# Kernel tuning notes

Measured on AMD Instinct MI355X. Metric: run time of the kernel, lower is better.

Reference implementation:

```python
import jax, jax.numpy as jnp
import numpy as np

N, E, D, L = 50000, 640000, 128, 3  # nodes, edges, channels, layers
EPS = 1e-5


def setup_inputs() -> dict:
    key = jax.random.key(0)
    ks = jax.random.split(key, 10)
    s = 1.0 / np.sqrt(D)
    inp = {
        "x": jax.random.normal(ks[0], (N, D), dtype=jnp.float32),
        "edge_attr": jax.random.normal(ks[1], (E, D), dtype=jnp.float32),
        "w_self": jax.random.normal(ks[2], (L, D, D), dtype=jnp.float32) * s,
        "b_self": jnp.zeros((L, D), dtype=jnp.float32),
        "w_in": jax.random.normal(ks[3], (L, D, D), dtype=jnp.float32) * s,
        "b_in": jnp.zeros((L, D), dtype=jnp.float32),
        "w_rel": jax.random.normal(ks[4], (L, D, D), dtype=jnp.float32) * s,
        "b_rel": jnp.zeros((L, D), dtype=jnp.float32),
        "bn_gamma": jnp.ones((L - 1, D), dtype=jnp.float32),
        "bn_beta": jnp.zeros((L - 1, D), dtype=jnp.float32),
        "edge_index": jax.random.randint(ks[5], (2, E), 0, N, dtype=jnp.int64),
    }
    return inp


def _batchnorm(h, gamma, beta):
    mu = jnp.mean(h, axis=0)
    var = jnp.mean(jnp.square(h - mu), axis=0)  # biased var (torch BN training)
    return (h - mu) * jax.lax.rsqrt(var + EPS) * gamma + beta


def reference(x, edge_attr, w_self, b_self, w_in, b_in, w_rel, b_rel,
              bn_gamma, bn_beta, edge_index):
    src, dst = edge_index[0], edge_index[1]
    # per-node in-degree for mean aggregation (zero-degree nodes -> 0)
    cnt = jax.ops.segment_sum(jnp.ones((E, 1), x.dtype), dst, num_segments=N)
    denom = jnp.maximum(cnt, 1.0)
    for i in range(L):
        # message: lin_in(x_j * edge_attr)
        msg = jnp.einsum('ed,fd->ef', x[src] * edge_attr, w_in[i]) + b_in[i]
        agg = jax.ops.segment_sum(msg, dst, num_segments=N) / denom  # scatter-mean
        x = agg + jnp.einsum('nd,fd->nf', x, w_self[i]) + b_self[i]
        edge_attr = jnp.einsum('ed,fd->ef', edge_attr, w_rel[i]) + b_rel[i]
        if i < L - 1:
            x = jax.nn.relu(_batchnorm(x, bn_gamma[i], bn_beta[i]))
            # dropout p=0.0 -> identity
    return (x, edge_attr)
```

## Files before the change

kernel.cpp:

```cpp
#include <hip/hip_runtime.h>

#define DD 128

typedef __attribute__((ext_vector_type(8))) short bf16x8;
typedef __attribute__((ext_vector_type(4))) short bf16x4;
typedef __attribute__((ext_vector_type(4))) float f32x4;
typedef unsigned short u16;

__device__ __forceinline__ unsigned short f2bf(float f) {
  union { float f; unsigned u; } v; v.f = f;
  unsigned u = v.u;
  return (unsigned short)((u + 0x7FFFu + ((u >> 16) & 1u)) >> 16);
}
__device__ __forceinline__ float bf2f(unsigned short h) {
  union { unsigned u; float f; } v; v.u = ((unsigned)h) << 16; return v.f;
}
__device__ __forceinline__ bf16x8 pack8(f32x4 a, f32x4 b) {
  bf16x8 r;
  r[0] = (short)f2bf(a.x); r[1] = (short)f2bf(a.y);
  r[2] = (short)f2bf(a.z); r[3] = (short)f2bf(a.w);
  r[4] = (short)f2bf(b.x); r[5] = (short)f2bf(b.y);
  r[6] = (short)f2bf(b.z); r[7] = (short)f2bf(b.w);
  return r;
}

__device__ __forceinline__ bool idx_is64(const int* p) {
  return (p[1] | p[3] | p[5] | p[7]) == 0;
}
__device__ __forceinline__ int ld_idx(const int* p, long long i, bool is64) {
  return is64 ? (int)((const long long*)p)[i] : p[i];
}

__global__ void k_count(const int* __restrict__ idx, int* __restrict__ cnt, int E) {
  int e = blockIdx.x * blockDim.x + threadIdx.x;
  if (e >= E) return;
  bool is64 = idx_is64(idx);
  int d = ld_idx(idx, (long long)E + e, is64);
  atomicAdd(&cnt[d], 1);
}

__global__ __launch_bounds__(1024) void k_scan(const int* __restrict__ cnt,
    int* __restrict__ row_start, int* __restrict__ cursor, int N) {
  __shared__ int part[1024];
  int t = threadIdx.x;
  int chunk = (N + 1023) >> 10;
  int lo = t * chunk, hi = lo + chunk; if (hi > N) hi = N; if (lo > N) lo = N;
  int s = 0;
  for (int i = lo; i < hi; ++i) s += cnt[i];
  part[t] = s;
  __syncthreads();
  for (int off = 1; off < 1024; off <<= 1) {
    int v = (t >= off) ? part[t - off] : 0;
    __syncthreads();
    part[t] += v;
    __syncthreads();
  }
  int run = (t == 0) ? 0 : part[t - 1];
  for (int i = lo; i < hi; ++i) {
    row_start[i] = run; cursor[i] = run; run += cnt[i];
  }
  if (t == 1023) row_start[N] = part[1023];
}

__global__ void k_fill(const int* __restrict__ idx, int* __restrict__ cursor,
                       int* __restrict__ edge_of, int* __restrict__ src_csr, int E) {
  int e = blockIdx.x * blockDim.x + threadIdx.x;
  if (e >= E) return;
  bool is64 = idx_is64(idx);
  int s = ld_idx(idx, e, is64);
  int d = ld_idx(idx, (long long)E + e, is64);
  int pos = atomicAdd(&cursor[d], 1);
  edge_of[pos] = e;
  src_csr[pos] = s;
}

template <int MODE>
__global__ __launch_bounds__(256, 4) void k_ar(
    const float* __restrict__ x0, const u16* __restrict__ xbin,
    const float* __restrict__ ea0, const u16* __restrict__ eain,
    u16* __restrict__ eabout, float* __restrict__ eafout,
    float* __restrict__ aggmf, u16* __restrict__ aggm,
    const int* __restrict__ row_start, const int* __restrict__ edge_of,
    const int* __restrict__ src_csr,
    const float* __restrict__ w_rel, const float* __restrict__ b_rel,
    const float* __restrict__ scale, const float* __restrict__ shift,
    int nA, int ntE) {
  __shared__ short Wl[16384];
  int bid = blockIdx.x;
  int tid = threadIdx.x;
  int wave = tid >> 6, lane = tid & 63;
  (void)aggmf;

  if (bid < nA) {
    int n = bid * 4 + wave;
    int esub = lane >> 4, cg = lane & 15;
    int c0 = cg * 8;
    float scA[8], shA[8];
    if constexpr (MODE >= 1) {
#pragma unroll
      for (int j = 0; j < 8; ++j) { scA[j] = scale[c0 + j]; shA[j] = shift[c0 + j]; }
    }
    int s0 = row_start[n], s1 = row_start[n + 1];
    int len = s1 - s0;
    float acc[8];
#pragma unroll
    for (int j = 0; j < 8; ++j) acc[j] = 0.f;
    for (int kk = 0; kk < len; kk += 8) {
      int kx0 = kk + esub, kx1 = kk + 4 + esub;
      bool a0 = kx0 < len, a1 = kx1 < len;
      int k0 = s0 + (a0 ? kx0 : 0);
      int k1 = s0 + (a1 ? kx1 : 0);
      if constexpr (MODE == 0) {
        int e0 = edge_of[k0], e1 = edge_of[k1];
        int sn0 = src_csr[k0], sn1 = src_csr[k1];
        const float* ep0 = ea0 + (size_t)e0 * DD + c0;
        const float* ep1 = ea0 + (size_t)e1 * DD + c0;
        const float* xp0 = x0 + (size_t)sn0 * DD + c0;
        const float* xp1 = x0 + (size_t)sn1 * DD + c0;
        f32x4 ea0a = *(const f32x4*)ep0, ea0b = *(const f32x4*)(ep0 + 4);
        f32x4 ea1a = *(const f32x4*)ep1, ea1b = *(const f32x4*)(ep1 + 4);
        f32x4 xv0a = *(const f32x4*)xp0, xv0b = *(const f32x4*)(xp0 + 4);
        f32x4 xv1a = *(const f32x4*)xp1, xv1b = *(const f32x4*)(xp1 + 4);
        if (a0) {
#pragma unroll
          for (int j = 0; j < 4; ++j) { acc[j] += xv0a[j] * ea0a[j]; acc[4 + j] += xv0b[j] * ea0b[j]; }
        }
        if (a1) {
#pragma unroll
          for (int j = 0; j < 4; ++j) { acc[j] += xv1a[j] * ea1a[j]; acc[4 + j] += xv1b[j] * ea1b[j]; }
        }
      } else {
        int sn0 = src_csr[k0], sn1 = src_csr[k1];
        bf16x8 ev0 = *(const bf16x8*)(eain + (size_t)k0 * DD + c0);
        bf16x8 ev1 = *(const bf16x8*)(eain + (size_t)k1 * DD + c0);
        bf16x8 xv0 = *(const bf16x8*)(xbin + (size_t)sn0 * DD + c0);
        bf16x8 xv1 = *(const bf16x8*)(xbin + (size_t)sn1 * DD + c0);
        if (a0) {
#pragma unroll
          for (int j = 0; j < 8; ++j) {
            float xf = fmaxf(bf2f((u16)xv0[j]) * scA[j] + shA[j], 0.f);
            acc[j] += xf * bf2f((u16)ev0[j]);
          }
        }
        if (a1) {
#pragma unroll
          for (int j = 0; j < 8; ++j) {
            float xf = fmaxf(bf2f((u16)xv1[j]) * scA[j] + shA[j], 0.f);
            acc[j] += xf * bf2f((u16)ev1[j]);
          }
        }
      }
    }
    float invd = (len > 0) ? 1.0f / (float)len : 0.0f;
#pragma unroll
    for (int j = 0; j < 8; ++j) {
      float s = acc[j];
      s += __shfl_xor(s, 16);
      s += __shfl_xor(s, 32);
      acc[j] = s * invd;
    }
    if (esub == 0) {
      f32x4 lo, hi;
#pragma unroll
      for (int j = 0; j < 4; ++j) { lo[j] = acc[j]; hi[j] = acc[4 + j]; }
      *(bf16x8*)(aggm + (size_t)n * DD + c0) = pack8(lo, hi);
    }
  } else {
    for (int q = tid; q < 4096; q += 256) {
      int off = q * 4;
      int f = off >> 7, d = off & 127;
      f32x4 w = *(const f32x4*)(w_rel + off);
      unsigned byte = ((unsigned)(f * 256 + d * 2)) ^ (unsigned)((f & 7) << 4);
      bf16x4 s4;
      s4[0] = (short)f2bf(w.x); s4[1] = (short)f2bf(w.y);
      s4[2] = (short)f2bf(w.z); s4[3] = (short)f2bf(w.w);
      *(bf16x4*)((char*)Wl + byte) = s4;
    }
    __syncthreads();
    int r = lane & 15, g = lane >> 4;
    int tile = (bid - nA) * 4 + wave;
    if (tile >= ntE) return;
    bf16x8 a8[4];
    if constexpr (MODE == 0) {
      int er = edge_of[tile * 16 + r];
      const float* rp = ea0 + (size_t)er * DD;
#pragma unroll
      for (int ks = 0; ks < 4; ++ks) {
        const float* p = rp + ks * 32 + g * 8;
        a8[ks] = pack8(*(const f32x4*)p, *(const f32x4*)(p + 4));
      }
    } else {
      const u16* rp = eain + (size_t)(tile * 16 + r) * DD;
#pragma unroll
      for (int ks = 0; ks < 4; ++ks) a8[ks] = *(const bf16x8*)(rp + ks * 32 + g * 8);
    }
    f32x4 acc4[8];
#pragma unroll
    for (int ct = 0; ct < 8; ++ct) acc4[ct] = (f32x4){0.f, 0.f, 0.f, 0.f};
#pragma unroll
    for (int ct = 0; ct < 8; ++ct) {
      int f = ct * 16 + r;
      unsigned base = (unsigned)(f * 256);
      unsigned sw = (unsigned)((f & 7) << 4);
#pragma unroll
      for (int ks = 0; ks < 4; ++ks) {
        unsigned byte = (base + (unsigned)(ks * 64 + g * 16)) ^ sw;
        bf16x8 bb = *(const bf16x8*)((const char*)Wl + byte);
        acc4[ct] = __builtin_amdgcn_mfma_f32_16x16x32_bf16(a8[ks], bb, acc4[ct], 0, 0, 0);
      }
    }
    size_t orow[4];
#pragma unroll
    for (int j = 0; j < 4; ++j) {
      int kr = tile * 16 + g * 4 + j;
      if constexpr (MODE == 2) orow[j] = (size_t)edge_of[kr];
      else                     orow[j] = (size_t)kr;
    }
#pragma unroll
    for (int ct = 0; ct < 8; ++ct) {
      int col = ct * 16 + r;
      float bv = b_rel[col];
#pragma unroll
      for (int j = 0; j < 4; ++j) {
        float v = acc4[ct][j] + bv;
        if constexpr (MODE == 2) eafout[orow[j] * DD + col] = v;
        else                     eabout[orow[j] * DD + col] = f2bf(v);
      }
    }
  }
}

template <typename TX, bool BN, typename TO, bool STATS>
__global__ __launch_bounds__(256, 2) void k_node(const u16* __restrict__ aggm,
    const TX* __restrict__ xc, const float* __restrict__ W_in,
    const float* __restrict__ W_self, const float* __restrict__ b_in,
    const float* __restrict__ b_self, const int* __restrict__ row_start,
    const float* __restrict__ scale, const float* __restrict__ shift,
    TO* __restrict__ xn, float* __restrict__ gsum, float* __restrict__ gssq,
    int ntiles) {
  __shared__ short Wl[DD * 256];
  for (int q = threadIdx.x; q < DD * 256 / 4; q += 256) {
    int off = q * 4;
    int f = off >> 8, k = off & 255;
    f32x4 w = (k < 128) ? *(const f32x4*)(W_in + f * 128 + k)
                        : *(const f32x4*)(W_self + f * 128 + (k - 128));
    unsigned byte = ((unsigned)(f * 512 + k * 2)) ^ (unsigned)((f & 7) << 4);
    bf16x4 s4;
    s4[0] = (short)f2bf(w.x); s4[1] = (short)f2bf(w.y);
    s4[2] = (short)f2bf(w.z); s4[3] = (short)f2bf(w.w);
    *(bf16x4*)((char*)Wl + byte) = s4;
  }
  __syncthreads();
  int wave = threadIdx.x >> 6, lane = threadIdx.x & 63;
  int tile = blockIdx.x * 4 + wave;
  if (tile >= ntiles) return;
  int r = lane & 15, g = lane >> 4;
  int arowi = tile * 16 + r;
  const u16* arow = aggm + (size_t)arowi * DD;
  const TX* xrow = xc + (size_t)arowi * DD;
  bf16x8 a[8];
#pragma unroll
  for (int ks = 0; ks < 4; ++ks) a[ks] = *(const bf16x8*)(arow + ks * 32 + g * 8);
#pragma unroll
  for (int ks = 0; ks < 4; ++ks) {
    int c0 = ks * 32 + g * 8;
    if constexpr (sizeof(TX) == 2) {
      bf16x8 raw = *(const bf16x8*)(xrow + c0);
      bf16x8 fr;
#pragma unroll
      for (int j = 0; j < 8; ++j) {
        float f = bf2f((u16)raw[j]);
        if constexpr (BN) f = fmaxf(f * scale[c0 + j] + shift[c0 + j], 0.f);
        fr[j] = (short)f2bf(f);
      }
      a[4 + ks] = fr;
    } else {
      const float* p = (const float*)xrow + c0;
      a[4 + ks] = pack8(*(const f32x4*)p, *(const f32x4*)(p + 4));
    }
  }
  f32x4 acc[8];
#pragma unroll
  for (int ct = 0; ct < 8; ++ct) acc[ct] = (f32x4){0.f, 0.f, 0.f, 0.f};
#pragma unroll
  for (int ct = 0; ct < 8; ++ct) {
    int f = ct * 16 + r;
    unsigned base = (unsigned)(f * 512);
    unsigned sw = (unsigned)((f & 7) << 4);
#pragma unroll
    for (int ks = 0; ks < 8; ++ks) {
      unsigned byte = (base + (unsigned)(ks * 64 + g * 16)) ^ sw;
      bf16x8 b = *(const bf16x8*)((const char*)Wl + byte);
      acc[ct] = __builtin_amdgcn_mfma_f32_16x16x32_bf16(a[ks], b, acc[ct], 0, 0, 0);
    }
  }
  int nbase = tile * 16;
  float degmask[4];
#pragma unroll
  for (int j = 0; j < 4; ++j) {
    int nn = nbase + g * 4 + j;
    degmask[j] = (row_start[nn + 1] > row_start[nn]) ? 1.0f : 0.0f;
  }
#pragma unroll
  for (int ct = 0; ct < 8; ++ct) {
    int col = ct * 16 + r;
    float bi = b_in[col], bs = b_self[col];
    float s = 0.f, s2 = 0.f;
#pragma unroll
    for (int j = 0; j < 4; ++j) {
      float v = acc[ct][j] + bs + bi * degmask[j];
      if constexpr (sizeof(TO) == 2) xn[(size_t)(nbase + g * 4 + j) * DD + col] = (TO)f2bf(v);
      else                            xn[(size_t)(nbase + g * 4 + j) * DD + col] = (TO)v;
      s += v; s2 += v * v;
    }
    if constexpr (STATS) {
      s += __shfl_xor(s, 16);  s += __shfl_xor(s, 32);
      s2 += __shfl_xor(s2, 16); s2 += __shfl_xor(s2, 32);
      if (g == 0) { atomicAdd(&gsum[col], s); atomicAdd(&gssq[col], s2); }
    }
  }
}

__global__ void k_bnfin(float* __restrict__ gsum, float* __restrict__ gssq,
    const float* __restrict__ gamma, const float* __restrict__ beta,
    float* __restrict__ scale, float* __restrict__ shift, int N) {
  int d = threadIdx.x;
  float mu = gsum[d] / (float)N;
  float var = gssq[d] / (float)N - mu * mu;
  float rs = rsqrtf(var + 1e-5f);
  float sc = rs * gamma[d];
  scale[d] = sc;
  shift[d] = beta[d] - mu * sc;
  gsum[d] = 0.f;
  gssq[d] = 0.f;
}

static inline size_t alignup(size_t v, size_t a) { return (v + a - 1) & ~(a - 1); }

extern "C" void kernel_launch(void* const* d_in, const int* in_sizes, int n_in,
                              void* d_out, int out_size, void* d_ws, size_t ws_size,
                              hipStream_t stream) {
  const float* x0     = (const float*)d_in[0];
  const float* ea0    = (const float*)d_in[1];
  const float* w_self = (const float*)d_in[2];
  const float* b_self = (const float*)d_in[3];
  const float* w_in   = (const float*)d_in[4];
  const float* b_in   = (const float*)d_in[5];
  const float* w_rel  = (const float*)d_in[6];
  const float* b_rel  = (const float*)d_in[7];
  const float* gamma  = (const float*)d_in[8];
  const float* beta   = (const float*)d_in[9];
  const int*   idx    = (const int*)d_in[10];

  const int N = in_sizes[0] / DD;
  const int E = in_sizes[1] / DD;

  char* w = (char*)d_ws;
  size_t off = 0;
  int* cnt       = (int*)(w + off); off = alignup(off + (size_t)N * 4, 256);
  int* row_start = (int*)(w + off); off = alignup(off + (size_t)(N + 1) * 4, 256);
  int* cursor    = (int*)(w + off); off = alignup(off + (size_t)N * 4, 256);
  int* edge_of   = (int*)(w + off); off = alignup(off + (size_t)E * 4, 256);
  int* src_csr   = (int*)(w + off); off = alignup(off + (size_t)E * 4, 256);
  float* gstats  = (float*)(w + off); off = alignup(off + 256 * 4, 256);
  float* scale   = (float*)(w + off); off = alignup(off + 128 * 4, 256);
  float* shift   = (float*)(w + off); off = alignup(off + 128 * 4, 256);
  u16* aggm      = (u16*)(w + off); off = alignup(off + (size_t)N * DD * 2, 256);
  u16* xbA       = (u16*)(w + off); off = alignup(off + (size_t)N * DD * 2, 256);
  u16* xbB       = (u16*)(w + off); off = alignup(off + (size_t)N * DD * 2, 256);
  u16* eaA       = (u16*)(w + off); off = alignup(off + (size_t)E * DD * 2, 256);
  u16* eaB       = (u16*)(w + off); off = alignup(off + (size_t)E * DD * 2, 256);
  float* gsum = gstats, *gssq = gstats + 128;
  (void)ws_size; (void)n_in; (void)out_size;

  float* out_x  = (float*)d_out;
  float* out_ea = out_x + (size_t)N * DD;

  (void)hipMemsetAsync(cnt, 0, (size_t)N * 4, stream);
  int ethreads = 256, eblocks = (E + ethreads - 1) / ethreads;
  k_count<<<eblocks, ethreads, 0, stream>>>(idx, cnt, E);
  k_scan<<<1, 1024, 0, stream>>>(cnt, row_start, cursor, N);
  k_fill<<<eblocks, ethreads, 0, stream>>>(idx, cursor, edge_of, src_csr, E);
  (void)hipMemsetAsync(gstats, 0, 256 * 4, stream);

  const int ntN = N / 16;
  const int ntE = E / 16;
  const int nA = (N + 3) / 4;
  const int nB = (ntE + 3) / 4;
  const int grid = nA + nB;
  const int nodeBlocks = (ntN + 3) / 4;

  k_ar<0><<<grid, 256, 0, stream>>>(x0, nullptr, ea0, nullptr,
      eaA, nullptr, nullptr, aggm, row_start, edge_of, src_csr,
      w_rel, b_rel, scale, shift, nA, ntE);
  k_node<float, false, u16, true><<<nodeBlocks, 256, 0, stream>>>(aggm, x0,
      w_in, w_self, b_in, b_self, row_start, scale, shift,
      xbA, gsum, gssq, ntN);
  k_bnfin<<<1, 128, 0, stream>>>(gsum, gssq, gamma, beta, scale, shift, N);

  k_ar<1><<<grid, 256, 0, stream>>>(nullptr, xbA, nullptr, eaA,
      eaB, nullptr, nullptr, aggm, row_start, edge_of, src_csr,
      w_rel + DD * DD, b_rel + DD, scale, shift, nA, ntE);
  k_node<u16, true, u16, true><<<nodeBlocks, 256, 0, stream>>>(aggm, xbA,
      w_in + DD * DD, w_self + DD * DD, b_in + DD, b_self + DD,
      row_start, scale, shift, xbB, gsum, gssq, ntN);
  k_bnfin<<<1, 128, 0, stream>>>(gsum, gssq, gamma + DD, beta + DD, scale, shift, N);

  k_ar<2><<<grid, 256, 0, stream>>>(nullptr, xbB, nullptr, eaB,
      nullptr, out_ea, nullptr, aggm, row_start, edge_of, src_csr,
      w_rel + 2 * DD * DD, b_rel + 2 * DD, scale, shift, nA, ntE);
  k_node<u16, true, float, false><<<nodeBlocks, 256, 0, stream>>>(aggm, xbB,
      w_in + 2 * DD * DD, w_self + 2 * DD * DD, b_in + 2 * DD, b_self + 2 * DD,
      row_start, scale, shift, out_x, gsum, gssq, ntN);
}
```

Measured before the change: 1.029 ms.

## Fuse edge aggregation into edge-update MFMA pass with segmented scan and atomics

Replaces the split node-gather / edge-GEMM kernel with a single edge-parallel kernel. Each wave loads an edge's attributes and source features once and uses them both for the w_rel MFMA and for the message product. Messages are reduced per destination with a segmented shuffle scan, written to an fp32 aggregation buffer with plain stores when a segment lies inside the wave's range and atomics otherwise. BatchNorm+ReLU moves into a separate elementwise pass that writes a post-activation bf16 copy. The cost is an extra fp32 N×D buffer that must be memset each layer, 32-float register carries and lower occupancy (launch bounds cut from 4 to 2), plus atomic contention on high-degree nodes.

```diff
diff --git a/kernel.cpp b/kernel.cpp
--- a/kernel.cpp
+++ b/kernel.cpp
@@ -63,7 +63,8 @@
 }
 
 __global__ void k_fill(const int* __restrict__ idx, int* __restrict__ cursor,
-                       int* __restrict__ edge_of, int* __restrict__ src_csr, int E) {
+                       int* __restrict__ edge_of, int* __restrict__ src_csr,
+                       int* __restrict__ dst_csr, int E) {
   int e = blockIdx.x * blockDim.x + threadIdx.x;
   if (e >= E) return;
   bool is64 = idx_is64(idx);
@@ -72,131 +73,82 @@
   int pos = atomicAdd(&cursor[d], 1);
   edge_of[pos] = e;
   src_csr[pos] = s;
+  dst_csr[pos] = d;
 }
 
 template <int MODE>
-__global__ __launch_bounds__(256, 4) void k_ar(
-    const float* __restrict__ x0, const u16* __restrict__ xbin,
+__global__ __launch_bounds__(256, 2) void k_layer(
+    const float* __restrict__ x0, const u16* __restrict__ xpin,
     const float* __restrict__ ea0, const u16* __restrict__ eain,
     u16* __restrict__ eabout, float* __restrict__ eafout,
-    float* __restrict__ aggmf, u16* __restrict__ aggm,
+    float* __restrict__ aggsum,
     const int* __restrict__ row_start, const int* __restrict__ edge_of,
-    const int* __restrict__ src_csr,
+    const int* __restrict__ src_csr, const int* __restrict__ dst_csr,
     const float* __restrict__ w_rel, const float* __restrict__ b_rel,
-    const float* __restrict__ scale, const float* __restrict__ shift,
-    int nA, int ntE) {
+    int E) {
   __shared__ short Wl[16384];
-  int bid = blockIdx.x;
-  int tid = threadIdx.x;
-  int wave = tid >> 6, lane = tid & 63;
-  (void)aggmf;
-
-  if (bid < nA) {
-    int n = bid * 4 + wave;
-    int esub = lane >> 4, cg = lane & 15;
-    int c0 = cg * 8;
-    float scA[8], shA[8];
-    if constexpr (MODE >= 1) {
-#pragma unroll
-      for (int j = 0; j < 8; ++j) { scA[j] = scale[c0 + j]; shA[j] = shift[c0 + j]; }
-    }
-    int s0 = row_start[n], s1 = row_start[n + 1];
-    int len = s1 - s0;
-    float acc[8];
-#pragma unroll
-    for (int j = 0; j < 8; ++j) acc[j] = 0.f;
-    for (int kk = 0; kk < len; kk += 8) {
-      int kx0 = kk + esub, kx1 = kk + 4 + esub;
-      bool a0 = kx0 < len, a1 = kx1 < len;
-      int k0 = s0 + (a0 ? kx0 : 0);
-      int k1 = s0 + (a1 ? kx1 : 0);
-      if constexpr (MODE == 0) {
-        int e0 = edge_of[k0], e1 = edge_of[k1];
-        int sn0 = src_csr[k0], sn1 = src_csr[k1];
-        const float* ep0 = ea0 + (size_t)e0 * DD + c0;
-        const float* ep1 = ea0 + (size_t)e1 * DD + c0;
-        const float* xp0 = x0 + (size_t)sn0 * DD + c0;
-        const float* xp1 = x0 + (size_t)sn1 * DD + c0;
-        f32x4 ea0a = *(const f32x4*)ep0, ea0b = *(const f32x4*)(ep0 + 4);
-        f32x4 ea1a = *(const f32x4*)ep1, ea1b = *(const f32x4*)(ep1 + 4);
-        f32x4 xv0a = *(const f32x4*)xp0, xv0b = *(const f32x4*)(xp0 + 4);
-        f32x4 xv1a = *(const f32x4*)xp1, xv1b = *(const f32x4*)(xp1 + 4);
-        if (a0) {
-#pragma unroll
-          for (int j = 0; j < 4; ++j) { acc[j] += xv0a[j] * ea0a[j]; acc[4 + j] += xv0b[j] * ea0b[j]; }
+  for (int q = threadIdx.x; q < 4096; q += 256) {
+    int off = q * 4;
+    int f = off >> 7, d = off & 127;
+    f32x4 w = *(const f32x4*)(w_rel + off);
+    unsigned byte = ((unsigned)(f * 256 + d * 2)) ^ (unsigned)((f & 7) << 4);
+    bf16x4 s4;
+    s4[0] = (short)f2bf(w.x); s4[1] = (short)f2bf(w.y);
+    s4[2] = (short)f2bf(w.z); s4[3] = (short)f2bf(w.w);
+    *(bf16x4*)((char*)Wl + byte) = s4;
+  }
+  __syncthreads();
+  int wid = blockIdx.x * 4 + (threadIdx.x >> 6);
+  int wk0 = wid * 64;
+  if (wk0 >= E) return;
+  int lane = threadIdx.x & 63, r = lane & 15, g = lane >> 4;
+
+  float carry[32];
+  int cdst = -1;
+#pragma unroll
+  for (int ch = 0; ch < 32; ++ch) carry[ch] = 0.f;
+
+#pragma unroll 1
+  for (int st = 0; st < 4; ++st) {
+    int k0 = wk0 + st * 16;
+    int kr = k0 + r;
+    int dr = dst_csr[kr];
+    int sn = src_csr[kr];
+    bf16x8 a8[4];
+    float m[32];
+    if constexpr (MODE == 0) {
+      int e = edge_of[kr];
+      const float* ep = ea0 + (size_t)e * DD;
+      const float* xp = x0 + (size_t)sn * DD;
+#pragma unroll
+      for (int ks = 0; ks < 4; ++ks) {
+        int c0 = ks * 32 + g * 8;
+        f32x4 e0 = *(const f32x4*)(ep + c0), e1 = *(const f32x4*)(ep + c0 + 4);
+        f32x4 xv0 = *(const f32x4*)(xp + c0), xv1 = *(const f32x4*)(xp + c0 + 4);
+        a8[ks] = pack8(e0, e1);
+#pragma unroll
+        for (int j = 0; j < 4; ++j) {
+          m[ks * 8 + j] = e0[j] * xv0[j];
+          m[ks * 8 + 4 + j] = e1[j] * xv1[j];
         }
-        if (a1) {
-#pragma unroll
-          for (int j = 0; j < 4; ++j) { acc[j] += xv1a[j] * ea1a[j]; acc[4 + j] += xv1b[j] * ea1b[j]; }
-        }
-      } else {
-        int sn0 = src_csr[k0], sn1 = src_csr[k1];
-        bf16x8 ev0 = *(const bf16x8*)(eain + (size_t)k0 * DD + c0);
-        bf16x8 ev1 = *(const bf16x8*)(eain + (size_t)k1 * DD + c0);
-        bf16x8 xv0 = *(const bf16x8*)(xbin + (size_t)sn0 * DD + c0);
-        bf16x8 xv1 = *(const bf16x8*)(xbin + (size_t)sn1 * DD + c0);
-        if (a0) {
-#pragma unroll
-          for (int j = 0; j < 8; ++j) {
-            float xf = fmaxf(bf2f((u16)xv0[j]) * scA[j] + shA[j], 0.f);
-            acc[j] += xf * bf2f((u16)ev0[j]);
-          }
-        }
-        if (a1) {
-#pragma unroll
-          for (int j = 0; j < 8; ++j) {
-            float xf = fmaxf(bf2f((u16)xv1[j]) * scA[j] + shA[j], 0.f);
-            acc[j] += xf * bf2f((u16)ev1[j]);
-          }
-        }
-      }
-    }
-    float invd = (len > 0) ? 1.0f / (float)len : 0.0f;
-#pragma unroll
-    for (int j = 0; j < 8; ++j) {
-      float s = acc[j];
-      s += __shfl_xor(s, 16);
-      s += __shfl_xor(s, 32);
-      acc[j] = s * invd;
-    }
-    if (esub == 0) {
-      f32x4 lo, hi;
-#pragma unroll
-      for (int j = 0; j < 4; ++j) { lo[j] = acc[j]; hi[j] = acc[4 + j]; }
-      *(bf16x8*)(aggm + (size_t)n * DD + c0) = pack8(lo, hi);
-    }
-  } else {
-    for (int q = tid; q < 4096; q += 256) {
-      int off = q * 4;
-      int f = off >> 7, d = off & 127;
-      f32x4 w = *(const f32x4*)(w_rel + off);
-      unsigned byte = ((unsigned)(f * 256 + d * 2)) ^ (unsigned)((f & 7) << 4);
-      bf16x4 s4;
-      s4[0] = (short)f2bf(w.x); s4[1] = (short)f2bf(w.y);
-      s4[2] = (short)f2bf(w.z); s4[3] = (short)f2bf(w.w);
-      *(bf16x4*)((char*)Wl + byte) = s4;
-    }
-    __syncthreads();
-    int r = lane & 15, g = lane >> 4;
-    int tile = (bid - nA) * 4 + wave;
-    if (tile >= ntE) return;
-    bf16x8 a8[4];
-    if constexpr (MODE == 0) {
-      int er = edge_of[tile * 16 + r];
-      const float* rp = ea0 + (size_t)er * DD;
+      }
+    } else {
+      const u16* ep = eain + (size_t)kr * DD;
+      const u16* xp = xpin + (size_t)sn * DD;
 #pragma unroll
       for (int ks = 0; ks < 4; ++ks) {
-        const float* p = rp + ks * 32 + g * 8;
-        a8[ks] = pack8(*(const f32x4*)p, *(const f32x4*)(p + 4));
-      }
-    } else {
-      const u16* rp = eain + (size_t)(tile * 16 + r) * DD;
-#pragma unroll
-      for (int ks = 0; ks < 4; ++ks) a8[ks] = *(const bf16x8*)(rp + ks * 32 + g * 8);
-    }
-    f32x4 acc4[8];
-#pragma unroll
-    for (int ct = 0; ct < 8; ++ct) acc4[ct] = (f32x4){0.f, 0.f, 0.f, 0.f};
+        int c0 = ks * 32 + g * 8;
+        bf16x8 ev = *(const bf16x8*)(ep + c0);
+        bf16x8 xv = *(const bf16x8*)(xp + c0);
+        a8[ks] = ev;
+#pragma unroll
+        for (int j = 0; j < 8; ++j)
+          m[ks * 8 + j] = bf2f((u16)ev[j]) * bf2f((u16)xv[j]);
+      }
+    }
+    f32x4 acc[8];
+#pragma unroll
+    for (int ct = 0; ct < 8; ++ct) acc[ct] = (f32x4){0.f, 0.f, 0.f, 0.f};
 #pragma unroll
     for (int ct = 0; ct < 8; ++ct) {
       int f = ct * 16 + r;
@@ -206,15 +158,15 @@
       for (int ks = 0; ks < 4; ++ks) {
         unsigned byte = (base + (unsigned)(ks * 64 + g * 16)) ^ sw;
         bf16x8 bb = *(const bf16x8*)((const char*)Wl + byte);
-        acc4[ct] = __builtin_amdgcn_mfma_f32_16x16x32_bf16(a8[ks], bb, acc4[ct], 0, 0, 0);
+        acc[ct] = __builtin_amdgcn_mfma_f32_16x16x32_bf16(a8[ks], bb, acc[ct], 0, 0, 0);
       }
     }
     size_t orow[4];
 #pragma unroll
     for (int j = 0; j < 4; ++j) {
-      int kr = tile * 16 + g * 4 + j;
-      if constexpr (MODE == 2) orow[j] = (size_t)edge_of[kr];
-      else                     orow[j] = (size_t)kr;
+      int kk = k0 + g * 4 + j;
+      if constexpr (MODE == 2) orow[j] = (size_t)edge_of[kk];
+      else                     orow[j] = (size_t)kk;
     }
 #pragma unroll
     for (int ct = 0; ct < 8; ++ct) {
@@ -222,20 +174,105 @@
       float bv = b_rel[col];
 #pragma unroll
       for (int j = 0; j < 4; ++j) {
-        float v = acc4[ct][j] + bv;
+        float v = acc[ct][j] + bv;
         if constexpr (MODE == 2) eafout[orow[j] * DD + col] = v;
         else                     eabout[orow[j] * DD + col] = f2bf(v);
       }
     }
-  }
-}
-
-template <typename TX, bool BN, typename TO, bool STATS>
-__global__ __launch_bounds__(256, 2) void k_node(const u16* __restrict__ aggm,
+    int d0 = __shfl(dr, 0, 16);
+    if (cdst >= 0 && cdst != d0) {
+      if (r == 0) {
+        int s0d = row_start[cdst], s1d = row_start[cdst + 1];
+        bool cont = (s0d >= wk0) && (s1d <= wk0 + 64);
+        float* dp = aggsum + (size_t)cdst * DD;
+        if (cont) {
+#pragma unroll
+          for (int ks = 0; ks < 4; ++ks) {
+            f32x4 lo, hi;
+#pragma unroll
+            for (int j = 0; j < 4; ++j) { lo[j] = carry[ks * 8 + j]; hi[j] = carry[ks * 8 + 4 + j]; }
+            *(f32x4*)(dp + ks * 32 + g * 8) = lo;
+            *(f32x4*)(dp + ks * 32 + g * 8 + 4) = hi;
+          }
+        } else {
+#pragma unroll
+          for (int ks = 0; ks < 4; ++ks)
+#pragma unroll
+            for (int j = 0; j < 8; ++j)
+              unsafeAtomicAdd(dp + ks * 32 + g * 8 + j, carry[ks * 8 + j]);
+        }
+      }
+      cdst = -1;
+    }
+#pragma unroll
+    for (int s = 1; s < 16; s <<= 1) {
+      int dprev = __shfl_up(dr, s, 16);
+      bool take = (r >= s) && (dprev == dr);
+#pragma unroll
+      for (int ch = 0; ch < 32; ++ch) {
+        float v = __shfl_up(m[ch], s, 16);
+        m[ch] += take ? v : 0.f;
+      }
+    }
+    if (dr == cdst) {
+#pragma unroll
+      for (int ch = 0; ch < 32; ++ch) m[ch] += carry[ch];
+    }
+    int dnext = __shfl_down(dr, 1, 16);
+    bool tail = (r < 15) && (dnext != dr);
+    if (tail) {
+      int s0d = row_start[dr], s1d = row_start[dr + 1];
+      bool cont = (s0d >= wk0) && (s1d <= wk0 + 64);
+      float* dp = aggsum + (size_t)dr * DD;
+      if (cont) {
+#pragma unroll
+        for (int ks = 0; ks < 4; ++ks) {
+          f32x4 lo, hi;
+#pragma unroll
+          for (int j = 0; j < 4; ++j) { lo[j] = m[ks * 8 + j]; hi[j] = m[ks * 8 + 4 + j]; }
+          *(f32x4*)(dp + ks * 32 + g * 8) = lo;
+          *(f32x4*)(dp + ks * 32 + g * 8 + 4) = hi;
+        }
+      } else {
+#pragma unroll
+        for (int ks = 0; ks < 4; ++ks)
+#pragma unroll
+          for (int j = 0; j < 8; ++j)
+            unsafeAtomicAdd(dp + ks * 32 + g * 8 + j, m[ks * 8 + j]);
+      }
+    }
+#pragma unroll
+    for (int ch = 0; ch < 32; ++ch) carry[ch] = __shfl(m[ch], 15, 16);
+    cdst = __shfl(dr, 15, 16);
+  }
+  if (cdst >= 0 && r == 0) {
+    int s0d = row_start[cdst], s1d = row_start[cdst + 1];
+    bool cont = (s0d >= wk0) && (s1d <= wk0 + 64);
+    float* dp = aggsum + (size_t)cdst * DD;
+    if (cont) {
+#pragma unroll
+      for (int ks = 0; ks < 4; ++ks) {
+        f32x4 lo, hi;
+#pragma unroll
+        for (int j = 0; j < 4; ++j) { lo[j] = carry[ks * 8 + j]; hi[j] = carry[ks * 8 + 4 + j]; }
+        *(f32x4*)(dp + ks * 32 + g * 8) = lo;
+        *(f32x4*)(dp + ks * 32 + g * 8 + 4) = hi;
+      }
+    } else {
+#pragma unroll
+      for (int ks = 0; ks < 4; ++ks)
+#pragma unroll
+        for (int j = 0; j < 8; ++j)
+          unsafeAtomicAdd(dp + ks * 32 + g * 8 + j, carry[ks * 8 + j]);
+    }
+  }
+}
+
+template <typename TX, typename TO, bool STATS>
+__global__ __launch_bounds__(256, 2) void k_node(const float* __restrict__ aggsum,
     const TX* __restrict__ xc, const float* __restrict__ W_in,
     const float* __restrict__ W_self, const float* __restrict__ b_in,
     const float* __restrict__ b_self, const int* __restrict__ row_start,
-    const float* __restrict__ scale, const float* __restrict__ shift,
     TO* __restrict__ xn, float* __restrict__ gsum, float* __restrict__ gssq,
     int ntiles) {
   __shared__ short Wl[DD * 256];
@@ -256,24 +293,23 @@
   if (tile >= ntiles) return;
   int r = lane & 15, g = lane >> 4;
   int arowi = tile * 16 + r;
-  const u16* arow = aggm + (size_t)arowi * DD;
+  int dr0 = row_start[arowi], dr1 = row_start[arowi + 1];
+  float inv = (dr1 > dr0) ? 1.0f / (float)(dr1 - dr0) : 0.0f;
+  const float* arow = aggsum + (size_t)arowi * DD;
   const TX* xrow = xc + (size_t)arowi * DD;
   bf16x8 a[8];
 #pragma unroll
-  for (int ks = 0; ks < 4; ++ks) a[ks] = *(const bf16x8*)(arow + ks * 32 + g * 8);
+  for (int ks = 0; ks < 4; ++ks) {
+    const float* p = arow + ks * 32 + g * 8;
+    f32x4 v0 = *(const f32x4*)p * inv;
+    f32x4 v1 = *(const f32x4*)(p + 4) * inv;
+    a[ks] = pack8(v0, v1);
+  }
 #pragma unroll
   for (int ks = 0; ks < 4; ++ks) {
     int c0 = ks * 32 + g * 8;
     if constexpr (sizeof(TX) == 2) {
-      bf16x8 raw = *(const bf16x8*)(xrow + c0);
-      bf16x8 fr;
-#pragma unroll
-      for (int j = 0; j < 8; ++j) {
-        float f = bf2f((u16)raw[j]);
-        if constexpr (BN) f = fmaxf(f * scale[c0 + j] + shift[c0 + j], 0.f);
-        fr[j] = (short)f2bf(f);
-      }
-      a[4 + ks] = fr;
+      a[4 + ks] = *(const bf16x8*)(xrow + c0);
     } else {
       const float* p = (const float*)xrow + c0;
       a[4 + ks] = pack8(*(const f32x4*)p, *(const f32x4*)(p + 4));
@@ -333,6 +369,22 @@
   shift[d] = beta[d] - mu * sc;
   gsum[d] = 0.f;
   gssq[d] = 0.f;
+}
+
+__global__ void k_bnapply(const u16* __restrict__ xb, u16* __restrict__ xpost,
+                          const float* __restrict__ scale,
+                          const float* __restrict__ shift, int total8) {
+  int i = blockIdx.x * blockDim.x + threadIdx.x;
+  if (i >= total8) return;
+  bf16x8 v = ((const bf16x8*)xb)[i];
+  int c0 = (i * 8) & 127;
+  bf16x8 o;
+#pragma unroll
+  for (int j = 0; j < 8; ++j) {
+    float f = fmaxf(bf2f((u16)v[j]) * scale[c0 + j] + shift[c0 + j], 0.f);
+    o[j] = (short)f2bf(f);
+  }
+  ((bf16x8*)xpost)[i] = o;
 }
 
 static inline size_t alignup(size_t v, size_t a) { return (v + a - 1) & ~(a - 1); }
@@ -362,12 +414,13 @@
   int* cursor    = (int*)(w + off); off = alignup(off + (size_t)N * 4, 256);
   int* edge_of   = (int*)(w + off); off = alignup(off + (size_t)E * 4, 256);
   int* src_csr   = (int*)(w + off); off = alignup(off + (size_t)E * 4, 256);
+  int* dst_csr   = (int*)(w + off); off = alignup(off + (size_t)E * 4, 256);
   float* gstats  = (float*)(w + off); off = alignup(off + 256 * 4, 256);
   float* scale   = (float*)(w + off); off = alignup(off + 128 * 4, 256);
   float* shift   = (float*)(w + off); off = alignup(off + 128 * 4, 256);
-  u16* aggm      = (u16*)(w + off); off = alignup(off + (size_t)N * DD * 2, 256);
+  float* aggsum  = (float*)(w + off); off = alignup(off + (size_t)N * DD * 4, 256);
   u16* xbA       = (u16*)(w + off); off = alignup(off + (size_t)N * DD * 2, 256);
-  u16* xbB       = (u16*)(w + off); off = alignup(off + (size_t)N * DD * 2, 256);
+  u16* xpost     = (u16*)(w + off); off = alignup(off + (size_t)N * DD * 2, 256);
   u16* eaA       = (u16*)(w + off); off = alignup(off + (size_t)E * DD * 2, 256);
   u16* eaB       = (u16*)(w + off); off = alignup(off + (size_t)E * DD * 2, 256);
   float* gsum = gstats, *gssq = gstats + 128;
@@ -380,36 +433,38 @@
   int ethreads = 256, eblocks = (E + ethreads - 1) / ethreads;
   k_count<<<eblocks, ethreads, 0, stream>>>(idx, cnt, E);
   k_scan<<<1, 1024, 0, stream>>>(cnt, row_start, cursor, N);
-  k_fill<<<eblocks, ethreads, 0, stream>>>(idx, cursor, edge_of, src_csr, E);
+  k_fill<<<eblocks, ethreads, 0, stream>>>(idx, cursor, edge_of, src_csr, dst_csr, E);
   (void)hipMemsetAsync(gstats, 0, 256 * 4, stream);
+  (void)hipMemsetAsync(aggsum, 0, (size_t)N * DD * 4, stream);
 
   const int ntN = N / 16;
-  const int ntE = E / 16;
-  const int nA = (N + 3) / 4;
-  const int nB = (ntE + 3) / 4;
-  const int grid = nA + nB;
   const int nodeBlocks = (ntN + 3) / 4;
-
-  k_ar<0><<<grid, 256, 0, stream>>>(x0, nullptr, ea0, nullptr,
-      eaA, nullptr, nullptr, aggm, row_start, edge_of, src_csr,
-      w_rel, b_rel, scale, shift, nA, ntE);
-  k_node<float, false, u16, true><<<nodeBlocks, 256, 0, stream>>>(aggm, x0,
-      w_in, w_self, b_in, b_self, row_start, scale, shift,
-      xbA, gsum, gssq, ntN);
+  const int layerBlocks = (E / 64 + 3) / 4;
+  const int bnBlocks = ((size_t)N * DD / 8 + 255) / 256;
+
+  k_layer<0><<<layerBlocks, 256, 0, stream>>>(x0, nullptr, ea0, nullptr,
+      eaA, nullptr, aggsum, row_start, edge_of, src_csr, dst_csr,
+      w_rel, b_rel, E);
+  k_node<float, u16, true><<<nodeBlocks, 256, 0, stream>>>(aggsum, x0,
+      w_in, w_self, b_in, b_self, row_start, xbA, gsum, gssq, ntN);
   k_bnfin<<<1, 128, 0, stream>>>(gsum, gssq, gamma, beta, scale, shift, N);
-
-  k_ar<1><<<grid, 256, 0, stream>>>(nullptr, xbA, nullptr, eaA,
-      eaB, nullptr, nullptr, aggm, row_start, edge_of, src_csr,
-      w_rel + DD * DD, b_rel + DD, scale, shift, nA, ntE);
-  k_node<u16, true, u16, true><<<nodeBlocks, 256, 0, stream>>>(aggm, xbA,
+  k_bnapply<<<bnBlocks, 256, 0, stream>>>(xbA, xpost, scale, shift, N * DD / 8);
+  (void)hipMemsetAsync(aggsum, 0, (size_t)N * DD * 4, stream);
+
+  k_layer<1><<<layerBlocks, 256, 0, stream>>>(nullptr, xpost, nullptr, eaA,
+      eaB, nullptr, aggsum, row_start, edge_of, src_csr, dst_csr,
+      w_rel + DD * DD, b_rel + DD, E);
+  k_node<u16, u16, true><<<nodeBlocks, 256, 0, stream>>>(aggsum, xpost,
       w_in + DD * DD, w_self + DD * DD, b_in + DD, b_self + DD,
-      row_start, scale, shift, xbB, gsum, gssq, ntN);
+      row_start, xbA, gsum, gssq, ntN);
   k_bnfin<<<1, 128, 0, stream>>>(gsum, gssq, gamma + DD, beta + DD, scale, shift, N);
-
-  k_ar<2><<<grid, 256, 0, stream>>>(nullptr, xbB, nullptr, eaB,
-      nullptr, out_ea, nullptr, aggm, row_start, edge_of, src_csr,
-      w_rel + 2 * DD * DD, b_rel + 2 * DD, scale, shift, nA, ntE);
-  k_node<u16, true, float, false><<<nodeBlocks, 256, 0, stream>>>(aggm, xbB,
+  k_bnapply<<<bnBlocks, 256, 0, stream>>>(xbA, xpost, scale, shift, N * DD / 8);
+  (void)hipMemsetAsync(aggsum, 0, (size_t)N * DD * 4, stream);
+
+  k_layer<2><<<layerBlocks, 256, 0, stream>>>(nullptr, xpost, nullptr, eaB,
+      nullptr, out_ea, aggsum, row_start, edge_of, src_csr, dst_csr,
+      w_rel + 2 * DD * DD, b_rel + 2 * DD, E);
+  k_node<u16, float, false><<<nodeBlocks, 256, 0, stream>>>(aggsum, xpost,
       w_in + 2 * DD * DD, w_self + 2 * DD * DD, b_in + 2 * DD, b_self + 2 * DD,
-      row_start, scale, shift, out_x, gsum, gssq, ntN);
-}
+      row_start, out_x, gsum, gssq, ntN);
+}
```

Result: slower. 1.148 ms (+11.5%).
